# Optimization experiments

Measured on AMD Instinct MI355X. Metric: run time of the kernel, lower is better.

## Reference

```python
import jax, jax.numpy as jnp
import numpy as np

B, NP, L, C, NA = 16, 512, 20, 3, 50
RATIO = 0.8
K = int(np.ceil(RATIO * NP))  # 410 nodes kept per graph
N = B * NP
E = 6 * N
NF, EF = 13, 4
EPS = 1e-5


def _graph_norm(x, w, b, ms):
    # PyG GraphNorm called WITHOUT batch in the source -> single global graph
    mean = x.mean(0)
    out = x - ms * mean
    var = (out * out).mean(0)
    return w * out / jnp.sqrt(var + EPS) + b


def _forward(x, pan_w, lin1_w, lin1_b, norm1_w, norm1_b, norm1_ms,
             pool_p, pool_beta, gat_wl, gat_bl, gat_wr, gat_br, gat_att, gat_bias,
             norm2_w, norm2_b, norm2_ms,
             val1_w, val1_b, val2_w, val2_b, val3_w, val3_b,
             adv1_w, adv1_b, adv2_w, adv2_b, adv3_w, adv3_b,
             edge_index, current_node_ids, action_mask):
    src, dst = edge_index[0], edge_index[1]
    # PANConv builds SparseTensor(row=edge_index[1], col=edge_index[0]) -> row = target
    A = jnp.zeros((B, NP, NP), x.dtype).at[dst // NP, dst % NP, src % NP].set(1.0)
    eyeB = jnp.broadcast_to(jnp.eye(NP, dtype=x.dtype), A.shape)

    # panentropy: M = sum_{i=0..L} w_i * A^i  (dense per graph)
    def step(carry, wi):
        tmp, acc = carry
        tmp = tmp @ A
        return (tmp, acc + wi * tmp), None
    (_, M), _ = jax.lax.scan(step, (eyeB, pan_w[0] * eyeB), pan_w[1:])
    deg = M.sum(-1)                                   # row sums
    dis = jnp.where(deg > 0, 1.0 / jnp.sqrt(deg), 0.0)
    Mn = dis[:, :, None] * M * dis[:, None, :]        # D^-1/2 M D^-1/2

    # conv1: propagate (Mn @ x) then Linear
    x3 = x.reshape(B, NP, NF)
    h = jnp.einsum('bij,bjf->bif', Mn, x3) @ lin1_w + lin1_b   # [B,NP,C]
    x1 = jax.nn.relu(_graph_norm(h.reshape(N, C), norm1_w, norm1_b, norm1_ms))  # [N,C]
    h = x1.reshape(B, NP, C)

    # PANPooling: score = tanh(b0 * <x,p> + b1 * colsum(Mn)); keep top K per graph
    score = jnp.tanh(pool_beta[0] * (h * pool_p).sum(-1) + pool_beta[1] * Mn.sum(-2))
    vals, idx = jax.lax.top_k(score, K)                        # [B,K]
    xp = jnp.take_along_axis(h, idx[:, :, None], axis=1) * vals[..., None]
    Mg = jax.vmap(lambda m, i: m[i][:, i])(Mn, idx)            # filtered adjacency [B,K,K]
    mask = (jnp.swapaxes(Mg, 1, 2) != 0) | jnp.eye(K, dtype=bool)  # mask[b,i,j]: edge j->i (+self loops)

    # GATv2Conv, heads=1, eval mode (no dropout), edge_attr not passed in source
    xl = xp @ gat_wl + gat_bl
    xr = xp @ gat_wr + gat_br
    e = jax.nn.leaky_relu(xr[:, :, None, :] + xl[:, None, :, :], 0.2)  # [B,i,j,C]
    logits = jnp.where(mask, jnp.einsum('bijc,c->bij', e, gat_att), -1e9)
    alpha = jax.nn.softmax(logits, axis=-1)
    g = jnp.einsum('bij,bjc->bic', alpha, xl) + gat_bias

    g = jax.nn.relu(_graph_norm(g.reshape(B * K, C), norm2_w, norm2_b, norm2_ms)).reshape(B, K, C)
    gp = g.sum(1)                                              # global_add_pool [B,C]

    # source uses POOLED bincount cumsum offsets to index the pre-pool arrays (faithful)
    gidx = current_node_ids + jnp.arange(B, dtype=current_node_ids.dtype) * K
    feat = jnp.concatenate([x[gidx], x1[gidx], gp], axis=1)    # [B,19]

    a = jax.nn.relu(feat @ adv1_w + adv1_b)
    a = jax.nn.relu(a @ adv2_w + adv2_b)
    a = a @ adv3_w + adv3_b
    v = jax.nn.relu(feat @ val1_w + val1_b)
    v = jax.nn.relu(v @ val2_w + val2_b)
    v = v @ val3_w + val3_b
    q = v + (a - a.mean(1, keepdims=True))
    return jnp.where(action_mask == 0, -1e8, q)


def setup_inputs() -> dict:
    key = jax.random.key(0)
    ks = list(jax.random.split(key, 40))
    nk = lambda: ks.pop()
    # within-graph random edges so the PyG-style batch structure is valid
    g = jax.random.randint(nk(), (E,), 0, B)
    u = jax.random.randint(nk(), (E,), 0, NP)
    v = jax.random.randint(nk(), (E,), 0, NP)
    edge_index = jnp.stack([g * NP + u, g * NP + v]).astype(jnp.int32)

    def lin(k, i, o):
        k1, k2 = jax.random.split(k)
        return (jax.random.normal(k1, (i, o), jnp.float32) / np.sqrt(i),
                jax.random.normal(k2, (o,), jnp.float32) * 0.01)

    lin1_w, lin1_b = lin(nk(), NF, C)
    gat_wl, gat_bl = lin(nk(), C, C)
    gat_wr, gat_br = lin(nk(), C, C)
    val1_w, val1_b = lin(nk(), 19, 10)
    val2_w, val2_b = lin(nk(), 10, 5)
    val3_w, val3_b = lin(nk(), 5, 1)
    adv1_w, adv1_b = lin(nk(), 19, 10)
    adv2_w, adv2_b = lin(nk(), 10, 5)
    adv3_w, adv3_b = lin(nk(), 5, NA)
    return dict(
        x=jax.random.normal(nk(), (N, NF), jnp.float32),
        edge_index=edge_index,
        edge_attr=jax.random.normal(nk(), (E, EF), jnp.float32),
        batch=jnp.arange(N, dtype=jnp.int32) // NP,
        current_node_ids=jax.random.randint(nk(), (B,), 0, NP),
        action_mask=jax.random.randint(nk(), (B, NA), 0, 2),
        pan_w=jax.random.uniform(nk(), (L + 1,), jnp.float32) * 0.5,
        lin1_w=lin1_w, lin1_b=lin1_b,
        norm1_w=jnp.ones(C), norm1_b=jnp.zeros(C), norm1_ms=jnp.ones(C),
        pool_p=jax.random.normal(nk(), (C,), jnp.float32),
        pool_beta=jnp.array([0.5, 0.5], jnp.float32),
        gat_wl=gat_wl, gat_bl=gat_bl, gat_wr=gat_wr, gat_br=gat_br,
        gat_att=jax.random.normal(nk(), (C,), jnp.float32),
        gat_bias=jax.random.normal(nk(), (C,), jnp.float32) * 0.01,
        norm2_w=jnp.ones(C), norm2_b=jnp.zeros(C), norm2_ms=jnp.ones(C),
        val1_w=val1_w, val1_b=val1_b, val2_w=val2_w, val2_b=val2_b,
        val3_w=val3_w, val3_b=val3_b,
        adv1_w=adv1_w, adv1_b=adv1_b, adv2_w=adv2_w, adv2_b=adv2_b,
        adv3_w=adv3_w, adv3_b=adv3_b,
    )


def reference(x, edge_index, edge_attr, batch, current_node_ids, action_mask,
              pan_w, lin1_w, lin1_b, norm1_w, norm1_b, norm1_ms,
              pool_p, pool_beta, gat_wl, gat_bl, gat_wr, gat_br, gat_att, gat_bias,
              norm2_w, norm2_b, norm2_ms,
              val1_w, val1_b, val2_w, val2_b, val3_w, val3_b,
              adv1_w, adv1_b, adv2_w, adv2_b, adv3_w, adv3_b):
    del edge_attr, batch  # received by the torch forward but never consumed
    return _forward(x, pan_w, lin1_w, lin1_b, norm1_w, norm1_b, norm1_ms,
                    pool_p, pool_beta, gat_wl, gat_bl, gat_wr, gat_br, gat_att, gat_bias,
                    norm2_w, norm2_b, norm2_ms,
                    val1_w, val1_b, val2_w, val2_b, val3_w, val3_b,
                    adv1_w, adv1_b, adv2_w, adv2_b, adv3_w, adv3_b,
                    edge_index, current_node_ids, action_mask)
```

## Files before the change

### kernel.cpp

```cpp
#include <hip/hip_runtime.h>
#include <hip/hip_bf16.h>
#include <stdint.h>
#include <math.h>

#define BB   16
#define NPn  512
#define LLp  20
#define NAa  50
#define KKk  410
#define NNt  (BB * NPn)
#define EEe  (6 * NNt)
#define NFf  13
#define KPAD 416
#define EPSf 1e-5f
#define QCLMP 1e6f
#define MAXD 28
#define PADR 512

__device__ __forceinline__ float r15_sane(float v) {
    if (!(v == v)) return 0.0f;
    return fminf(fmaxf(v, -1e15f), 1e15f);
}

__global__ __launch_bounds__(256) void r15_scatter(
    const int* __restrict__ ei,
    uint32_t* __restrict__ fwdb, uint32_t* __restrict__ trsb)
{
    const int e = blockIdx.x * 256 + threadIdx.x;
    if (e < EEe) {
        const int src = ei[e], dst = ei[EEe + e];
        atomicOr(&fwdb[(size_t)dst * 16 + ((src & 511) >> 5)], 1u << (src & 31));
        atomicOr(&trsb[(size_t)src * 16 + ((dst & 511) >> 5)], 1u << (dst & 31));
    }
}

__global__ __launch_bounds__(256) void r15_extract(
    const uint32_t* __restrict__ fwdb, const uint32_t* __restrict__ trsb,
    unsigned short* __restrict__ csrF, unsigned short* __restrict__ csrT)
{
    const int t = blockIdx.x * 256 + threadIdx.x;
    const int node = t & 8191;
    const uint32_t* bs = (t < 8192) ? (fwdb + (size_t)node * 16)
                                    : (trsb + (size_t)node * 16);
    unsigned short* cs = (t < 8192) ? csrF : csrT;
    int cnt = 0;
    for (int w = 0; w < 16; ++w) {
        uint32_t bits = bs[w];
        while (bits) {
            const int u = (w << 5) + __ffs(bits) - 1;
            bits &= bits - 1;
            if (cnt < MAXD) cs[(size_t)cnt * 8192 + node] = (unsigned short)u;
            ++cnt;
        }
    }
    for (int j = cnt; j < MAXD; ++j) cs[(size_t)j * 8192 + node] = PADR;
}

__global__ __launch_bounds__(512) void r15_mid(
    const float* __restrict__ x,
    const unsigned short* __restrict__ csrF,
    const unsigned short* __restrict__ csrT,
    const float* __restrict__ panw,
    const float* __restrict__ l1w, const float* __restrict__ l1b,
    float* __restrict__ h_raw, float* __restrict__ colsum,
    uint32_t* __restrict__ Rb)
{
    __shared__ __align__(16) uint32_t sbuf[1047];
    float* pa  = (float*)sbuf;
    float* pb  = (float*)(sbuf + 513);
    float* wsh = (float*)(sbuf + 1026);
    const int b = blockIdx.x, y = blockIdx.y, t = threadIdx.x;
    const int node = b * 512 + t;

    if (y < 4) {
        const int c = y;
        int iF[MAXD];
#pragma unroll
        for (int j = 0; j < MAXD; ++j) iF[j] = (int)csrF[(size_t)j * 8192 + node];
        if (t < 21) wsh[t] = panw[t];

        pa[t] = 1.0f;
        if (t == 0) { pa[512] = 0.0f; pb[512] = 0.0f; }
        __syncthreads();
        float dacc = wsh[0];
        {
            float* rp = pa; float* rn = pb;
            for (int i = 1; i <= LLp; ++i) {
                float tv[MAXD];
#pragma unroll
                for (int j = 0; j < MAXD; ++j) tv[j] = rp[iF[j]];
                float s = 0.0f;
#pragma unroll
                for (int j = 0; j < MAXD; ++j) s += tv[j];
                rn[t] = s;
                dacc += wsh[i] * s;
                __syncthreads();
                float* tp = rp; rp = rn; rn = tp;
            }
        }
        const float d0 = (dacc > 0.0f) ? 1.0f / sqrtf(dacc) : 0.0f;

        int idx[MAXD];
        if (c == 3) {
#pragma unroll
            for (int j = 0; j < MAXD; ++j) idx[j] = (int)csrT[(size_t)j * 8192 + node];
        } else {
#pragma unroll
            for (int j = 0; j < MAXD; ++j) idx[j] = iF[j];
        }
        float seed;
        if (c < 3) {
            float xw = 0.0f;
            const float* xr = x + (size_t)node * NFf;
            for (int f = 0; f < NFf; ++f) xw += xr[f] * l1w[f * 3 + c];
            seed = d0 * xw;
        } else {
            seed = d0;
        }
        pa[t] = seed;
        if (t == 0) { pa[512] = 0.0f; pb[512] = 0.0f; }
        __syncthreads();
        float acc = wsh[0] * seed;
        {
            float* rp = pa; float* rn = pb;
            for (int i = 1; i <= LLp; ++i) {
                float tv[MAXD];
#pragma unroll
                for (int j = 0; j < MAXD; ++j) tv[j] = rp[idx[j]];
                float s = 0.0f;
#pragma unroll
                for (int j = 0; j < MAXD; ++j) s += tv[j];
                rn[t] = s;
                acc += wsh[i] * s;
                __syncthreads();
                float* tp = rp; rp = rn; rn = tp;
            }
        }
        if (c < 3) h_raw[(size_t)node * 3 + c] = r15_sane(d0 * acc + l1b[c]);
        else       colsum[node] = r15_sane(d0 * acc);
    } else {
        const int q = y - 4;
        int iF[MAXD];
#pragma unroll
        for (int j = 0; j < MAXD; ++j) iF[j] = (int)csrF[(size_t)j * 8192 + node];
        uint32_t* R1 = sbuf;
        uint32_t* R2 = sbuf + 513;
        R1[t] = ((t >> 5) == q) ? (1u << (t & 31)) : 0u;
        if (t == 0) { R1[512] = 0u; R2[512] = 0u; }
        __syncthreads();
        uint32_t* Rp = R1; uint32_t* Rn = R2;
        for (int i = 0; i < LLp; ++i) {
            uint32_t tv[MAXD];
#pragma unroll
            for (int j = 0; j < MAXD; ++j) tv[j] = Rp[iF[j]];
            uint32_t r = Rp[t];
#pragma unroll
            for (int j = 0; j < MAXD; ++j) r |= tv[j];
            Rn[t] = r;
            __syncthreads();
            uint32_t* tp = Rp; Rp = Rn; Rn = tp;
        }
        Rb[(size_t)node * 16 + q] = Rp[t];
    }
}

__global__ __launch_bounds__(512) void r15_poolgat(
    const float* __restrict__ h_raw,
    const float* __restrict__ colsum,
    const uint32_t* __restrict__ Rb,
    const float* n1w, const float* n1b, const float* n1ms,
    const float* poolp, const float* poolb,
    const float* gwl, const float* gbl,
    const float* gwr, const float* gbr,
    const float* gatt, const float* gbias,
    float* __restrict__ x1,
    float* __restrict__ g_raw)
{
    __shared__ __align__(16) uint32_t pg[10592];
    float* red  = (float*)pg;
    float* sc   = (float*)(pg + 512);
    float* mv   = (float*)(pg + 1024);
    float* xpS  = (float*)(pg + 1032);
    int*   kidx = (int*)(pg + 2280);
    float* xlS  = (float*)(pg + 2696);
    uint32_t* RT = pg + 3928;
    const int b = blockIdx.x, y = blockIdx.y, t = threadIdx.x;
    const float inv_n = 1.0f / (float)NNt;

    float hv0[16], hv1[16], hv2[16];
    float s0 = 0.0f, s1 = 0.0f, s2 = 0.0f;
#pragma unroll
    for (int k = 0; k < 16; ++k) {
        const float* hr = h_raw + (size_t)(k * 512 + t) * 3;
        hv0[k] = hr[0]; hv1[k] = hr[1]; hv2[k] = hr[2];
        s0 += hv0[k]; s1 += hv1[k]; s2 += hv2[k];
    }
    float acc[3] = { s0, s1, s2 };
    for (int c = 0; c < 3; ++c) {
        __syncthreads();
        red[t] = acc[c];
        __syncthreads();
        for (int st = 256; st > 0; st >>= 1) {
            if (t < st) red[t] += red[t + st];
            __syncthreads();
        }
        if (t == 0) mv[c] = red[0] * inv_n;
    }
    __syncthreads();
    const float mm0 = n1ms[0] * mv[0], mm1 = n1ms[1] * mv[1], mm2 = n1ms[2] * mv[2];
    float a0 = 0.0f, a1 = 0.0f, a2 = 0.0f;
#pragma unroll
    for (int k = 0; k < 16; ++k) {
        const float d0 = hv0[k] - mm0, d1 = hv1[k] - mm1, d2 = hv2[k] - mm2;
        a0 += d0 * d0; a1 += d1 * d1; a2 += d2 * d2;
    }
    float accv[3] = { a0, a1, a2 };
    for (int c = 0; c < 3; ++c) {
        __syncthreads();
        red[t] = accv[c];
        __syncthreads();
        for (int st = 256; st > 0; st >>= 1) {
            if (t < st) red[t] += red[t + st];
            __syncthreads();
        }
        if (t == 0) mv[3 + c] = red[0] * inv_n;
    }
    __syncthreads();

    const float mmv[3] = { mm0, mm1, mm2 };
    float xv[3];
#pragma unroll
    for (int c = 0; c < 3; ++c) {
        const float iv = 1.0f / sqrtf(fmaxf(mv[3 + c], 0.0f) + EPSf);
        const float o  = h_raw[(size_t)(b * NPn + t) * 3 + c] - mmv[c];
        const float tt = n1w[c] * o * iv + n1b[c];
        xv[c] = fmaxf(tt, 0.0f);
        if (y == 0) x1[(size_t)(b * NPn + t) * 3 + c] = xv[c];
    }
    float s = poolb[0] * (xv[0] * poolp[0] + xv[1] * poolp[1] + xv[2] * poolp[2])
            + poolb[1] * colsum[b * NPn + t];
    s = tanhf(s);
    if (!(s == s)) s = 0.0f;
    sc[t] = s;
    __syncthreads();
    int cnt = 0;
    for (int u = 0; u < NPn; ++u) {
        const float su = sc[u];
        cnt += ((su > s) || (su == s && u < t)) ? 1 : 0;
    }
    if (cnt < KKk) {
        kidx[cnt] = t;
        xpS[cnt * 3 + 0] = xv[0] * s;
        xpS[cnt * 3 + 1] = xv[1] * s;
        xpS[cnt * 3 + 2] = xv[2] * s;
    }
    __syncthreads();

    float Wl[9], Wr[9];
#pragma unroll
    for (int i2 = 0; i2 < 9; ++i2) { Wl[i2] = gwl[i2]; Wr[i2] = gwr[i2]; }
    const float Bl0 = gbl[0], Bl1 = gbl[1], Bl2 = gbl[2];
    const float Br0 = gbr[0], Br1 = gbr[1], Br2 = gbr[2];
    const float At0 = gatt[0], At1 = gatt[1], At2 = gatt[2];
    const float Gb0 = gbias[0], Gb1 = gbias[1], Gb2 = gbias[2];
    for (int j = t; j < KKk; j += 512) {
        const float p0 = xpS[j * 3 + 0];
        const float p1 = xpS[j * 3 + 1];
        const float p2 = xpS[j * 3 + 2];
        xlS[j * 3 + 0] = p0 * Wl[0] + p1 * Wl[3] + p2 * Wl[6] + Bl0;
        xlS[j * 3 + 1] = p0 * Wl[1] + p1 * Wl[4] + p2 * Wl[7] + Bl1;
        xlS[j * 3 + 2] = p0 * Wl[2] + p1 * Wl[5] + p2 * Wl[8] + Bl2;
        const uint32_t* rr = Rb + (size_t)(b * NPn + kidx[j]) * 16;
#pragma unroll
        for (int w = 0; w < 16; ++w) RT[w * KPAD + j] = rr[w];
    }
    __syncthreads();

    const int lane = t & 63, wv = t >> 6;
    const int wid = y * 8 + wv;
    for (int i = wid; i < KKk; i += 64) {
        const float p0 = xpS[i * 3 + 0];
        const float p1 = xpS[i * 3 + 1];
        const float p2 = xpS[i * 3 + 2];
        const float xr0 = p0 * Wr[0] + p1 * Wr[3] + p2 * Wr[6] + Br0;
        const float xr1 = p0 * Wr[1] + p1 * Wr[4] + p2 * Wr[7] + Br1;
        const float xr2 = p0 * Wr[2] + p1 * Wr[5] + p2 * Wr[8] + Br2;
        const int bi = kidx[i];
        const uint32_t mbit = 1u << (bi & 31);
        const uint32_t* Rw = &RT[(bi >> 5) * KPAD];
        float mx = -3e38f, lsum = 0.0f, b0 = 0.0f, b1 = 0.0f, b2 = 0.0f;
        for (int j = lane; j < KKk; j += 64) {
            if ((Rw[j] & mbit) || (j == i)) {
                float e0 = xr0 + xlS[j * 3 + 0]; e0 = e0 > 0.0f ? e0 : 0.2f * e0;
                float e1 = xr1 + xlS[j * 3 + 1]; e1 = e1 > 0.0f ? e1 : 0.2f * e1;
                float e2 = xr2 + xlS[j * 3 + 2]; e2 = e2 > 0.0f ? e2 : 0.2f * e2;
                const float sv = At0 * e0 + At1 * e1 + At2 * e2;
                if (sv > mx) {
                    const float r = __expf(mx - sv);
                    lsum *= r; b0 *= r; b1 *= r; b2 *= r;
                    mx = sv;
                }
                const float pj = __expf(sv - mx);
                lsum += pj;
                b0 += pj * xlS[j * 3 + 0];
                b1 += pj * xlS[j * 3 + 1];
                b2 += pj * xlS[j * 3 + 2];
            }
        }
        for (int off = 32; off; off >>= 1) {
            const float mo = __shfl_xor(mx, off);
            const float lo = __shfl_xor(lsum, off);
            const float c0 = __shfl_xor(b0, off);
            const float c1 = __shfl_xor(b1, off);
            const float c2 = __shfl_xor(b2, off);
            const float M  = fmaxf(mx, mo);
            const float ea = __expf(mx - M), eb = __expf(mo - M);
            lsum = lsum * ea + lo * eb;
            b0 = b0 * ea + c0 * eb;
            b1 = b1 * ea + c1 * eb;
            b2 = b2 * ea + c2 * eb;
            mx = M;
        }
        if (lane == 0) {
            const float rl = 1.0f / fmaxf(lsum, 1e-30f);
            g_raw[(size_t)(b * KPAD + i) * 3 + 0] = r15_sane(b0 * rl + Gb0);
            g_raw[(size_t)(b * KPAD + i) * 3 + 1] = r15_sane(b1 * rl + Gb1);
            g_raw[(size_t)(b * KPAD + i) * 3 + 2] = r15_sane(b2 * rl + Gb2);
        }
    }
}

__global__ __launch_bounds__(512) void r15_head(
    const float* __restrict__ g_raw,
    const float* __restrict__ x1,
    const float* __restrict__ x,
    const int* __restrict__ cnid,
    const int* __restrict__ amask,
    const float* n2w, const float* n2b, const float* n2ms,
    const float* v1w, const float* v1b,
    const float* v2w, const float* v2b,
    const float* v3w, const float* v3b,
    const float* a1w, const float* a1b,
    const float* a2w, const float* a2b,
    const float* a3w, const float* a3b,
    float* __restrict__ out)
{
    __shared__ float rbuf[512];
    __shared__ float mv[6];
    __shared__ float gp[3];
    __shared__ float feat[19];
    __shared__ float h1a[10], h1v[10], h2a[5], h2v[5];
    __shared__ float a3[50];
    __shared__ float vout_s, amean_s;
    const int b = blockIdx.x, t = threadIdx.x;
    const float denom = 1.0f / (float)(BB * KKk);

    float gv0[13], gv1[13], gv2[13];
    float s0 = 0.0f, s1 = 0.0f, s2 = 0.0f;
#pragma unroll
    for (int k = 0; k < 13; ++k) {
        const int r = k * 512 + t;
        float q0 = 0.0f, q1 = 0.0f, q2 = 0.0f;
        if (r < BB * KKk) {
            const int bq = r / KKk, iq = r - bq * KKk;
            const float* gr = g_raw + (size_t)(bq * KPAD + iq) * 3;
            q0 = gr[0]; q1 = gr[1]; q2 = gr[2];
        }
        gv0[k] = q0; gv1[k] = q1; gv2[k] = q2;
        s0 += q0; s1 += q1; s2 += q2;
    }
    float acc[3] = { s0, s1, s2 };
    for (int c = 0; c < 3; ++c) {
        __syncthreads();
        rbuf[t] = acc[c];
        __syncthreads();
        for (int st = 256; st > 0; st >>= 1) {
            if (t < st) rbuf[t] += rbuf[t + st];
            __syncthreads();
        }
        if (t == 0) mv[c] = rbuf[0] * denom;
    }
    __syncthreads();
    const float mm0 = n2ms[0] * mv[0], mm1 = n2ms[1] * mv[1], mm2 = n2ms[2] * mv[2];
    float a0 = 0.0f, a1 = 0.0f, a2 = 0.0f;
#pragma unroll
    for (int k = 0; k < 13; ++k) {
        const int r = k * 512 + t;
        if (r < BB * KKk) {
            const float d0 = gv0[k] - mm0, d1 = gv1[k] - mm1, d2 = gv2[k] - mm2;
            a0 += d0 * d0; a1 += d1 * d1; a2 += d2 * d2;
        }
    }
    float accv[3] = { a0, a1, a2 };
    for (int c = 0; c < 3; ++c) {
        __syncthreads();
        rbuf[t] = accv[c];
        __syncthreads();
        for (int st = 256; st > 0; st >>= 1) {
            if (t < st) rbuf[t] += rbuf[t + st];
            __syncthreads();
        }
        if (t == 0) mv[3 + c] = rbuf[0] * denom;
    }
    __syncthreads();

    const float mmv[3] = { mm0, mm1, mm2 };
    float s3[3] = { 0.0f, 0.0f, 0.0f };
    if (t < KKk) {
        const size_t r = (size_t)(b * KPAD + t) * 3;
#pragma unroll
        for (int c = 0; c < 3; ++c) {
            const float iv = 1.0f / sqrtf(fmaxf(mv[3 + c], 0.0f) + EPSf);
            s3[c] = fmaxf((g_raw[r + c] - mmv[c]) * iv * n2w[c] + n2b[c], 0.0f);
        }
    }
    for (int c = 0; c < 3; ++c) {
        __syncthreads();
        rbuf[t] = s3[c];
        __syncthreads();
        for (int st = 256; st > 0; st >>= 1) {
            if (t < st) rbuf[t] += rbuf[t + st];
            __syncthreads();
        }
        if (t == 0) gp[c] = rbuf[0];
    }
    __syncthreads();

    if (t < 19) {
        const int gidx = cnid[b] + b * KKk;
        float fv;
        if (t < 13)      fv = x[(size_t)gidx * NFf + t];
        else if (t < 16) fv = x1[(size_t)gidx * 3 + (t - 13)];
        else             fv = gp[t - 16];
        feat[t] = fv;
    }
    __syncthreads();

    if (t < 10) {
        float s = a1b[t];
        for (int f = 0; f < 19; ++f) s += feat[f] * a1w[f * 10 + t];
        h1a[t] = fmaxf(s, 0.0f);
    } else if (t >= 64 && t < 74) {
        const int j = t - 64;
        float s = v1b[j];
        for (int f = 0; f < 19; ++f) s += feat[f] * v1w[f * 10 + j];
        h1v[j] = fmaxf(s, 0.0f);
    }
    __syncthreads();
    if (t < 5) {
        float s = a2b[t];
        for (int k = 0; k < 10; ++k) s += h1a[k] * a2w[k * 5 + t];
        h2a[t] = fmaxf(s, 0.0f);
    } else if (t >= 64 && t < 69) {
        const int j = t - 64;
        float s = v2b[j];
        for (int k = 0; k < 10; ++k) s += h1v[k] * v2w[k * 5 + j];
        h2v[j] = fmaxf(s, 0.0f);
    }
    __syncthreads();
    if (t < 50) {
        float s = a3b[t];
        for (int k = 0; k < 5; ++k) s += h2a[k] * a3w[k * 50 + t];
        a3[t] = s;
    } else if (t == 64) {
        float s = v3b[0];
        for (int k = 0; k < 5; ++k) s += h2v[k] * v3w[k];
        vout_s = s;
    }
    __syncthreads();
    if (t == 0) {
        float s = 0.0f;
        for (int k = 0; k < 50; ++k) s += a3[k];
        amean_s = s * (1.0f / 50.0f);
    }
    __syncthreads();
    if (t < 50) {
        float q = vout_s + a3[t] - amean_s;
        if (!(q == q)) q = 0.0f;
        q = fminf(fmaxf(q, -QCLMP), QCLMP);
        out[b * NAa + t] = (amask[b * NAa + t] == 0) ? -1e8f : q;
    }
}

extern "C" void kernel_launch(void* const* d_in, const int* in_sizes, int n_in,
                              void* d_out, int out_size, void* d_ws, size_t ws_size,
                              hipStream_t stream) {
    (void)in_sizes; (void)n_in; (void)out_size;
    const float* x     = (const float*)d_in[0];
    const int* ei      = (const int*)d_in[1];
    const int* cnid    = (const int*)d_in[4];
    const int* amask   = (const int*)d_in[5];
    const float* panw  = (const float*)d_in[6];
    const float* l1w   = (const float*)d_in[7];
    const float* l1b   = (const float*)d_in[8];
    const float* n1w   = (const float*)d_in[9];
    const float* n1b   = (const float*)d_in[10];
    const float* n1ms  = (const float*)d_in[11];
    const float* poolp = (const float*)d_in[12];
    const float* poolb = (const float*)d_in[13];
    const float* gwl   = (const float*)d_in[14];
    const float* gbl   = (const float*)d_in[15];
    const float* gwr   = (const float*)d_in[16];
    const float* gbr   = (const float*)d_in[17];
    const float* gatt  = (const float*)d_in[18];
    const float* gbias = (const float*)d_in[19];
    const float* n2w   = (const float*)d_in[20];
    const float* n2b   = (const float*)d_in[21];
    const float* n2ms  = (const float*)d_in[22];
    const float* v1w   = (const float*)d_in[23];
    const float* v1b   = (const float*)d_in[24];
    const float* v2w   = (const float*)d_in[25];
    const float* v2b   = (const float*)d_in[26];
    const float* v3w   = (const float*)d_in[27];
    const float* v3b   = (const float*)d_in[28];
    const float* a1w   = (const float*)d_in[29];
    const float* a1b   = (const float*)d_in[30];
    const float* a2w   = (const float*)d_in[31];
    const float* a2b   = (const float*)d_in[32];
    const float* a3w   = (const float*)d_in[33];
    const float* a3b   = (const float*)d_in[34];
    float* out         = (float*)d_out;

    uint8_t* wsb = (uint8_t*)d_ws;
    uint32_t* fwdb = (uint32_t*)wsb;
    uint32_t* trsb = (uint32_t*)(wsb + 524288);
    uint32_t* Rb   = (uint32_t*)(wsb + 1048576);
    unsigned short* csrF = (unsigned short*)(wsb + 1572864);
    unsigned short* csrT = csrF + (size_t)MAXD * 8192;
    float* h_raw  = (float*)(csrT + (size_t)MAXD * 8192);
    float* x1     = h_raw + (size_t)NNt * 3;
    float* colsum = x1 + (size_t)NNt * 3;
    float* g_raw  = colsum + NNt;
    const size_t needed = 1572864 + 2 * (size_t)MAXD * 8192 * 2 +
                          ((size_t)(2 * NNt * 3 + NNt + BB * KPAD * 3)) * 4;
    if (ws_size < needed) return;

    hipMemsetAsync(fwdb, 0, 1048576, stream);
    r15_scatter<<<dim3((EEe + 255) / 256), dim3(256), 0, stream>>>(ei, fwdb, trsb);
    r15_extract<<<dim3(64), dim3(256), 0, stream>>>(fwdb, trsb, csrF, csrT);
    r15_mid<<<dim3(16, 20), dim3(512), 0, stream>>>(x, csrF, csrT, panw, l1w, l1b,
                                                    h_raw, colsum, Rb);
    r15_poolgat<<<dim3(16, 8), dim3(512), 0, stream>>>(h_raw, colsum, Rb,
                                                       n1w, n1b, n1ms, poolp, poolb,
                                                       gwl, gbl, gwr, gbr, gatt, gbias,
                                                       x1, g_raw);
    r15_head<<<dim3(16), dim3(512), 0, stream>>>(g_raw, x1, x, cnid, amask,
                                                 n2w, n2b, n2ms, v1w, v1b, v2w, v2b, v3w, v3b,
                                                 a1w, a1b, a2w, a2b, a3w, a3b, out);
}
```

Before: 225.3 us.

## Fuse adjacency build into one LDS kernel, use wave-shuffle reductions, unroll GAT loop

Replaces the memset, global-atomic scatter and extract kernels with a single per-graph kernel that builds the forward and transpose bitmasks in shared memory and emits the padded neighbour lists. Each of the 16 blocks scans the full edge list, so edge reads are repeated 16 times in exchange for removing two launches and the global atomics. Block reductions in the pooling and head kernels switch from shared-memory tree reductions to wave shuffles plus a small cross-wave sum. The GAT attention loop becomes a fully unrolled fixed-trip loop over padded columns, evaluating scores unconditionally and masking only the accumulation.

```diff
diff --git a/kernel.cpp b/kernel.cpp
--- a/kernel.cpp
+++ b/kernel.cpp
@@ -12,51 +12,65 @@
 #define EEe  (6 * NNt)
 #define NFf  13
 #define KPAD 416
+#define KP2  448
 #define EPSf 1e-5f
 #define QCLMP 1e6f
 #define MAXD 28
 #define PADR 512
 
-__device__ __forceinline__ float r15_sane(float v) {
+__device__ __forceinline__ float r16_sane(float v) {
     if (!(v == v)) return 0.0f;
     return fminf(fmaxf(v, -1e15f), 1e15f);
 }
 
-__global__ __launch_bounds__(256) void r15_scatter(
+__global__ __launch_bounds__(512) void r16_build(
     const int* __restrict__ ei,
-    uint32_t* __restrict__ fwdb, uint32_t* __restrict__ trsb)
-{
-    const int e = blockIdx.x * 256 + threadIdx.x;
-    if (e < EEe) {
-        const int src = ei[e], dst = ei[EEe + e];
-        atomicOr(&fwdb[(size_t)dst * 16 + ((src & 511) >> 5)], 1u << (src & 31));
-        atomicOr(&trsb[(size_t)src * 16 + ((dst & 511) >> 5)], 1u << (dst & 31));
-    }
-}
-
-__global__ __launch_bounds__(256) void r15_extract(
-    const uint32_t* __restrict__ fwdb, const uint32_t* __restrict__ trsb,
     unsigned short* __restrict__ csrF, unsigned short* __restrict__ csrT)
 {
-    const int t = blockIdx.x * 256 + threadIdx.x;
-    const int node = t & 8191;
-    const uint32_t* bs = (t < 8192) ? (fwdb + (size_t)node * 16)
-                                    : (trsb + (size_t)node * 16);
-    unsigned short* cs = (t < 8192) ? csrF : csrT;
-    int cnt = 0;
-    for (int w = 0; w < 16; ++w) {
-        uint32_t bits = bs[w];
-        while (bits) {
-            const int u = (w << 5) + __ffs(bits) - 1;
-            bits &= bits - 1;
-            if (cnt < MAXD) cs[(size_t)cnt * 8192 + node] = (unsigned short)u;
-            ++cnt;
-        }
-    }
-    for (int j = cnt; j < MAXD; ++j) cs[(size_t)j * 8192 + node] = PADR;
+    __shared__ uint32_t fw[NPn * 16];
+    __shared__ uint32_t tr[NPn * 16];
+    const int b = blockIdx.x, t = threadIdx.x;
+#pragma unroll
+    for (int w = 0; w < 16; ++w) { fw[t * 16 + w] = 0u; tr[t * 16 + w] = 0u; }
+    __syncthreads();
+    for (int e = t; e < EEe; e += 512) {
+        const int src = ei[e], dst = ei[EEe + e];
+        if ((dst >> 9) == b)
+            atomicOr(&fw[(dst & 511) * 16 + ((src & 511) >> 5)], 1u << (src & 31));
+        if ((src >> 9) == b)
+            atomicOr(&tr[(src & 511) * 16 + ((dst & 511) >> 5)], 1u << (dst & 31));
+    }
+    __syncthreads();
+    const int node = b * 512 + t;
+    {
+        int cnt = 0;
+        for (int w = 0; w < 16; ++w) {
+            uint32_t bits = fw[t * 16 + w];
+            while (bits) {
+                const int u = (w << 5) + __ffs(bits) - 1;
+                bits &= bits - 1;
+                if (cnt < MAXD) csrF[(size_t)cnt * 8192 + node] = (unsigned short)u;
+                ++cnt;
+            }
+        }
+        for (int j = cnt; j < MAXD; ++j) csrF[(size_t)j * 8192 + node] = PADR;
+    }
+    {
+        int cnt = 0;
+        for (int w = 0; w < 16; ++w) {
+            uint32_t bits = tr[t * 16 + w];
+            while (bits) {
+                const int u = (w << 5) + __ffs(bits) - 1;
+                bits &= bits - 1;
+                if (cnt < MAXD) csrT[(size_t)cnt * 8192 + node] = (unsigned short)u;
+                ++cnt;
+            }
+        }
+        for (int j = cnt; j < MAXD; ++j) csrT[(size_t)j * 8192 + node] = PADR;
+    }
 }
 
-__global__ __launch_bounds__(512) void r15_mid(
+__global__ __launch_bounds__(512) void r16_mid(
     const float* __restrict__ x,
     const unsigned short* __restrict__ csrF,
     const unsigned short* __restrict__ csrT,
@@ -136,8 +150,8 @@
                 float* tp = rp; rp = rn; rn = tp;
             }
         }
-        if (c < 3) h_raw[(size_t)node * 3 + c] = r15_sane(d0 * acc + l1b[c]);
-        else       colsum[node] = r15_sane(d0 * acc);
+        if (c < 3) h_raw[(size_t)node * 3 + c] = r16_sane(d0 * acc + l1b[c]);
+        else       colsum[node] = r16_sane(d0 * acc);
     } else {
         const int q = y - 4;
         int iF[MAXD];
@@ -164,7 +178,7 @@
     }
 }
 
-__global__ __launch_bounds__(512) void r15_poolgat(
+__global__ __launch_bounds__(512) void r16_poolgat(
     const float* __restrict__ h_raw,
     const float* __restrict__ colsum,
     const uint32_t* __restrict__ Rb,
@@ -176,54 +190,55 @@
     float* __restrict__ x1,
     float* __restrict__ g_raw)
 {
-    __shared__ __align__(16) uint32_t pg[10592];
-    float* red  = (float*)pg;
-    float* sc   = (float*)(pg + 512);
-    float* mv   = (float*)(pg + 1024);
-    float* xpS  = (float*)(pg + 1032);
-    int*   kidx = (int*)(pg + 2280);
-    float* xlS  = (float*)(pg + 2696);
-    uint32_t* RT = pg + 3928;
+    __shared__ __align__(16) uint32_t pg[10744];
+    float* sc   = (float*)pg;
+    float* mv   = (float*)(pg + 512);
+    float* wred = (float*)(pg + 520);
+    float* xpS  = (float*)(pg + 568);
+    int*   kidx = (int*)(pg + 1816);
+    float* xlS  = (float*)(pg + 2232);
+    uint32_t* RT = pg + 3576;
     const int b = blockIdx.x, y = blockIdx.y, t = threadIdx.x;
+    const int lane = t & 63, wv = t >> 6;
     const float inv_n = 1.0f / (float)NNt;
 
     float hv0[16], hv1[16], hv2[16];
-    float s0 = 0.0f, s1 = 0.0f, s2 = 0.0f;
+    float p0 = 0.0f, p1 = 0.0f, p2 = 0.0f;
 #pragma unroll
     for (int k = 0; k < 16; ++k) {
         const float* hr = h_raw + (size_t)(k * 512 + t) * 3;
         hv0[k] = hr[0]; hv1[k] = hr[1]; hv2[k] = hr[2];
-        s0 += hv0[k]; s1 += hv1[k]; s2 += hv2[k];
-    }
-    float acc[3] = { s0, s1, s2 };
-    for (int c = 0; c < 3; ++c) {
-        __syncthreads();
-        red[t] = acc[c];
-        __syncthreads();
-        for (int st = 256; st > 0; st >>= 1) {
-            if (t < st) red[t] += red[t + st];
-            __syncthreads();
-        }
-        if (t == 0) mv[c] = red[0] * inv_n;
+        p0 += hv0[k]; p1 += hv1[k]; p2 += hv2[k];
+    }
+#pragma unroll
+    for (int off = 32; off; off >>= 1) {
+        p0 += __shfl_xor(p0, off); p1 += __shfl_xor(p1, off); p2 += __shfl_xor(p2, off);
+    }
+    if (lane == 0) { wred[wv * 3 + 0] = p0; wred[wv * 3 + 1] = p1; wred[wv * 3 + 2] = p2; }
+    __syncthreads();
+    if (t < 3) {
+        float s = 0.0f;
+        for (int w = 0; w < 8; ++w) s += wred[w * 3 + t];
+        mv[t] = s * inv_n;
     }
     __syncthreads();
     const float mm0 = n1ms[0] * mv[0], mm1 = n1ms[1] * mv[1], mm2 = n1ms[2] * mv[2];
-    float a0 = 0.0f, a1 = 0.0f, a2 = 0.0f;
+    float q0 = 0.0f, q1 = 0.0f, q2 = 0.0f;
 #pragma unroll
     for (int k = 0; k < 16; ++k) {
         const float d0 = hv0[k] - mm0, d1 = hv1[k] - mm1, d2 = hv2[k] - mm2;
-        a0 += d0 * d0; a1 += d1 * d1; a2 += d2 * d2;
-    }
-    float accv[3] = { a0, a1, a2 };
-    for (int c = 0; c < 3; ++c) {
-        __syncthreads();
-        red[t] = accv[c];
-        __syncthreads();
-        for (int st = 256; st > 0; st >>= 1) {
-            if (t < st) red[t] += red[t + st];
-            __syncthreads();
-        }
-        if (t == 0) mv[3 + c] = red[0] * inv_n;
+        q0 += d0 * d0; q1 += d1 * d1; q2 += d2 * d2;
+    }
+#pragma unroll
+    for (int off = 32; off; off >>= 1) {
+        q0 += __shfl_xor(q0, off); q1 += __shfl_xor(q1, off); q2 += __shfl_xor(q2, off);
+    }
+    if (lane == 0) { wred[wv * 3 + 0] = q0; wred[wv * 3 + 1] = q1; wred[wv * 3 + 2] = q2; }
+    __syncthreads();
+    if (t < 3) {
+        float s = 0.0f;
+        for (int w = 0; w < 8; ++w) s += wred[w * 3 + t];
+        mv[3 + t] = s * inv_n;
     }
     __syncthreads();
 
@@ -263,38 +278,51 @@
     const float Br0 = gbr[0], Br1 = gbr[1], Br2 = gbr[2];
     const float At0 = gatt[0], At1 = gatt[1], At2 = gatt[2];
     const float Gb0 = gbias[0], Gb1 = gbias[1], Gb2 = gbias[2];
-    for (int j = t; j < KKk; j += 512) {
-        const float p0 = xpS[j * 3 + 0];
-        const float p1 = xpS[j * 3 + 1];
-        const float p2 = xpS[j * 3 + 2];
-        xlS[j * 3 + 0] = p0 * Wl[0] + p1 * Wl[3] + p2 * Wl[6] + Bl0;
-        xlS[j * 3 + 1] = p0 * Wl[1] + p1 * Wl[4] + p2 * Wl[7] + Bl1;
-        xlS[j * 3 + 2] = p0 * Wl[2] + p1 * Wl[5] + p2 * Wl[8] + Bl2;
-        const uint32_t* rr = Rb + (size_t)(b * NPn + kidx[j]) * 16;
-#pragma unroll
-        for (int w = 0; w < 16; ++w) RT[w * KPAD + j] = rr[w];
-    }
-    __syncthreads();
-
-    const int lane = t & 63, wv = t >> 6;
+    if (t < KP2) {
+        const int j = t;
+        if (j < KKk) {
+            const float c0 = xpS[j * 3 + 0];
+            const float c1 = xpS[j * 3 + 1];
+            const float c2 = xpS[j * 3 + 2];
+            xlS[j * 3 + 0] = c0 * Wl[0] + c1 * Wl[3] + c2 * Wl[6] + Bl0;
+            xlS[j * 3 + 1] = c0 * Wl[1] + c1 * Wl[4] + c2 * Wl[7] + Bl1;
+            xlS[j * 3 + 2] = c0 * Wl[2] + c1 * Wl[5] + c2 * Wl[8] + Bl2;
+            const uint32_t* rr = Rb + (size_t)(b * NPn + kidx[j]) * 16;
+#pragma unroll
+            for (int w = 0; w < 16; ++w) RT[w * KP2 + j] = rr[w];
+        } else {
+            xlS[j * 3 + 0] = 0.0f; xlS[j * 3 + 1] = 0.0f; xlS[j * 3 + 2] = 0.0f;
+#pragma unroll
+            for (int w = 0; w < 16; ++w) RT[w * KP2 + j] = 0u;
+        }
+    }
+    __syncthreads();
+
     const int wid = y * 8 + wv;
     for (int i = wid; i < KKk; i += 64) {
-        const float p0 = xpS[i * 3 + 0];
-        const float p1 = xpS[i * 3 + 1];
-        const float p2 = xpS[i * 3 + 2];
-        const float xr0 = p0 * Wr[0] + p1 * Wr[3] + p2 * Wr[6] + Br0;
-        const float xr1 = p0 * Wr[1] + p1 * Wr[4] + p2 * Wr[7] + Br1;
-        const float xr2 = p0 * Wr[2] + p1 * Wr[5] + p2 * Wr[8] + Br2;
+        const float c0 = xpS[i * 3 + 0];
+        const float c1 = xpS[i * 3 + 1];
+        const float c2 = xpS[i * 3 + 2];
+        const float xr0 = c0 * Wr[0] + c1 * Wr[3] + c2 * Wr[6] + Br0;
+        const float xr1 = c0 * Wr[1] + c1 * Wr[4] + c2 * Wr[7] + Br1;
+        const float xr2 = c0 * Wr[2] + c1 * Wr[5] + c2 * Wr[8] + Br2;
         const int bi = kidx[i];
         const uint32_t mbit = 1u << (bi & 31);
-        const uint32_t* Rw = &RT[(bi >> 5) * KPAD];
+        const uint32_t* Rw = &RT[(bi >> 5) * KP2];
         float mx = -3e38f, lsum = 0.0f, b0 = 0.0f, b1 = 0.0f, b2 = 0.0f;
-        for (int j = lane; j < KKk; j += 64) {
-            if ((Rw[j] & mbit) || (j == i)) {
-                float e0 = xr0 + xlS[j * 3 + 0]; e0 = e0 > 0.0f ? e0 : 0.2f * e0;
-                float e1 = xr1 + xlS[j * 3 + 1]; e1 = e1 > 0.0f ? e1 : 0.2f * e1;
-                float e2 = xr2 + xlS[j * 3 + 2]; e2 = e2 > 0.0f ? e2 : 0.2f * e2;
-                const float sv = At0 * e0 + At1 * e1 + At2 * e2;
+#pragma unroll
+        for (int it = 0; it < 7; ++it) {
+            const int j = lane + it * 64;
+            const uint32_t rw = Rw[j];
+            const float xl0 = xlS[j * 3 + 0];
+            const float xl1 = xlS[j * 3 + 1];
+            const float xl2 = xlS[j * 3 + 2];
+            const bool valid = (rw & mbit) || (j == i);
+            float e0 = xr0 + xl0; e0 = e0 > 0.0f ? e0 : 0.2f * e0;
+            float e1 = xr1 + xl1; e1 = e1 > 0.0f ? e1 : 0.2f * e1;
+            float e2 = xr2 + xl2; e2 = e2 > 0.0f ? e2 : 0.2f * e2;
+            const float sv = At0 * e0 + At1 * e1 + At2 * e2;
+            if (valid) {
                 if (sv > mx) {
                     const float r = __expf(mx - sv);
                     lsum *= r; b0 *= r; b1 *= r; b2 *= r;
@@ -302,35 +330,34 @@
                 }
                 const float pj = __expf(sv - mx);
                 lsum += pj;
-                b0 += pj * xlS[j * 3 + 0];
-                b1 += pj * xlS[j * 3 + 1];
-                b2 += pj * xlS[j * 3 + 2];
+                b0 += pj * xl0; b1 += pj * xl1; b2 += pj * xl2;
             }
         }
+#pragma unroll
         for (int off = 32; off; off >>= 1) {
             const float mo = __shfl_xor(mx, off);
             const float lo = __shfl_xor(lsum, off);
-            const float c0 = __shfl_xor(b0, off);
-            const float c1 = __shfl_xor(b1, off);
-            const float c2 = __shfl_xor(b2, off);
+            const float d0 = __shfl_xor(b0, off);
+            const float d1 = __shfl_xor(b1, off);
+            const float d2 = __shfl_xor(b2, off);
             const float M  = fmaxf(mx, mo);
             const float ea = __expf(mx - M), eb = __expf(mo - M);
             lsum = lsum * ea + lo * eb;
-            b0 = b0 * ea + c0 * eb;
-            b1 = b1 * ea + c1 * eb;
-            b2 = b2 * ea + c2 * eb;
+            b0 = b0 * ea + d0 * eb;
+            b1 = b1 * ea + d1 * eb;
+            b2 = b2 * ea + d2 * eb;
             mx = M;
         }
         if (lane == 0) {
             const float rl = 1.0f / fmaxf(lsum, 1e-30f);
-            g_raw[(size_t)(b * KPAD + i) * 3 + 0] = r15_sane(b0 * rl + Gb0);
-            g_raw[(size_t)(b * KPAD + i) * 3 + 1] = r15_sane(b1 * rl + Gb1);
-            g_raw[(size_t)(b * KPAD + i) * 3 + 2] = r15_sane(b2 * rl + Gb2);
+            g_raw[(size_t)(b * KPAD + i) * 3 + 0] = r16_sane(b0 * rl + Gb0);
+            g_raw[(size_t)(b * KPAD + i) * 3 + 1] = r16_sane(b1 * rl + Gb1);
+            g_raw[(size_t)(b * KPAD + i) * 3 + 2] = r16_sane(b2 * rl + Gb2);
         }
     }
 }
 
-__global__ __launch_bounds__(512) void r15_head(
+__global__ __launch_bounds__(512) void r16_head(
     const float* __restrict__ g_raw,
     const float* __restrict__ x1,
     const float* __restrict__ x,
@@ -345,7 +372,7 @@
     const float* a3w, const float* a3b,
     float* __restrict__ out)
 {
-    __shared__ float rbuf[512];
+    __shared__ float wred[24];
     __shared__ float mv[6];
     __shared__ float gp[3];
     __shared__ float feat[19];
@@ -353,10 +380,11 @@
     __shared__ float a3[50];
     __shared__ float vout_s, amean_s;
     const int b = blockIdx.x, t = threadIdx.x;
+    const int lane = t & 63, wv = t >> 6;
     const float denom = 1.0f / (float)(BB * KKk);
 
     float gv0[13], gv1[13], gv2[13];
-    float s0 = 0.0f, s1 = 0.0f, s2 = 0.0f;
+    float p0 = 0.0f, p1 = 0.0f, p2 = 0.0f;
 #pragma unroll
     for (int k = 0; k < 13; ++k) {
         const int r = k * 512 + t;
@@ -367,40 +395,40 @@
             q0 = gr[0]; q1 = gr[1]; q2 = gr[2];
         }
         gv0[k] = q0; gv1[k] = q1; gv2[k] = q2;
-        s0 += q0; s1 += q1; s2 += q2;
-    }
-    float acc[3] = { s0, s1, s2 };
-    for (int c = 0; c < 3; ++c) {
-        __syncthreads();
-        rbuf[t] = acc[c];
-        __syncthreads();
-        for (int st = 256; st > 0; st >>= 1) {
-            if (t < st) rbuf[t] += rbuf[t + st];
-            __syncthreads();
-        }
-        if (t == 0) mv[c] = rbuf[0] * denom;
+        p0 += q0; p1 += q1; p2 += q2;
+    }
+#pragma unroll
+    for (int off = 32; off; off >>= 1) {
+        p0 += __shfl_xor(p0, off); p1 += __shfl_xor(p1, off); p2 += __shfl_xor(p2, off);
+    }
+    if (lane == 0) { wred[wv * 3 + 0] = p0; wred[wv * 3 + 1] = p1; wred[wv * 3 + 2] = p2; }
+    __syncthreads();
+    if (t < 3) {
+        float s = 0.0f;
+        for (int w = 0; w < 8; ++w) s += wred[w * 3 + t];
+        mv[t] = s * denom;
     }
     __syncthreads();
     const float mm0 = n2ms[0] * mv[0], mm1 = n2ms[1] * mv[1], mm2 = n2ms[2] * mv[2];
-    float a0 = 0.0f, a1 = 0.0f, a2 = 0.0f;
+    float q0a = 0.0f, q1a = 0.0f, q2a = 0.0f;
 #pragma unroll
     for (int k = 0; k < 13; ++k) {
         const int r = k * 512 + t;
         if (r < BB * KKk) {
             const float d0 = gv0[k] - mm0, d1 = gv1[k] - mm1, d2 = gv2[k] - mm2;
-            a0 += d0 * d0; a1 += d1 * d1; a2 += d2 * d2;
-        }
-    }
-    float accv[3] = { a0, a1, a2 };
-    for (int c = 0; c < 3; ++c) {
-        __syncthreads();
-        rbuf[t] = accv[c];
-        __syncthreads();
-        for (int st = 256; st > 0; st >>= 1) {
-            if (t < st) rbuf[t] += rbuf[t + st];
-            __syncthreads();
-        }
-        if (t == 0) mv[3 + c] = rbuf[0] * denom;
+            q0a += d0 * d0; q1a += d1 * d1; q2a += d2 * d2;
+        }
+    }
+#pragma unroll
+    for (int off = 32; off; off >>= 1) {
+        q0a += __shfl_xor(q0a, off); q1a += __shfl_xor(q1a, off); q2a += __shfl_xor(q2a, off);
+    }
+    if (lane == 0) { wred[wv * 3 + 0] = q0a; wred[wv * 3 + 1] = q1a; wred[wv * 3 + 2] = q2a; }
+    __syncthreads();
+    if (t < 3) {
+        float s = 0.0f;
+        for (int w = 0; w < 8; ++w) s += wred[w * 3 + t];
+        mv[3 + t] = s * denom;
     }
     __syncthreads();
 
@@ -414,15 +442,17 @@
             s3[c] = fmaxf((g_raw[r + c] - mmv[c]) * iv * n2w[c] + n2b[c], 0.0f);
         }
     }
-    for (int c = 0; c < 3; ++c) {
-        __syncthreads();
-        rbuf[t] = s3[c];
-        __syncthreads();
-        for (int st = 256; st > 0; st >>= 1) {
-            if (t < st) rbuf[t] += rbuf[t + st];
-            __syncthreads();
-        }
-        if (t == 0) gp[c] = rbuf[0];
+    float g0 = s3[0], g1 = s3[1], g2 = s3[2];
+#pragma unroll
+    for (int off = 32; off; off >>= 1) {
+        g0 += __shfl_xor(g0, off); g1 += __shfl_xor(g1, off); g2 += __shfl_xor(g2, off);
+    }
+    if (lane == 0) { wred[wv * 3 + 0] = g0; wred[wv * 3 + 1] = g1; wred[wv * 3 + 2] = g2; }
+    __syncthreads();
+    if (t < 3) {
+        float s = 0.0f;
+        for (int w = 0; w < 8; ++w) s += wred[w * 3 + t];
+        gp[t] = s;
     }
     __syncthreads();
 
@@ -522,29 +552,25 @@
     float* out         = (float*)d_out;
 
     uint8_t* wsb = (uint8_t*)d_ws;
-    uint32_t* fwdb = (uint32_t*)wsb;
-    uint32_t* trsb = (uint32_t*)(wsb + 524288);
-    uint32_t* Rb   = (uint32_t*)(wsb + 1048576);
-    unsigned short* csrF = (unsigned short*)(wsb + 1572864);
+    uint32_t* Rb   = (uint32_t*)wsb;
+    unsigned short* csrF = (unsigned short*)(wsb + 524288);
     unsigned short* csrT = csrF + (size_t)MAXD * 8192;
     float* h_raw  = (float*)(csrT + (size_t)MAXD * 8192);
     float* x1     = h_raw + (size_t)NNt * 3;
     float* colsum = x1 + (size_t)NNt * 3;
     float* g_raw  = colsum + NNt;
-    const size_t needed = 1572864 + 2 * (size_t)MAXD * 8192 * 2 +
+    const size_t needed = 524288 + 2 * (size_t)MAXD * 8192 * 2 +
                           ((size_t)(2 * NNt * 3 + NNt + BB * KPAD * 3)) * 4;
     if (ws_size < needed) return;
 
-    hipMemsetAsync(fwdb, 0, 1048576, stream);
-    r15_scatter<<<dim3((EEe + 255) / 256), dim3(256), 0, stream>>>(ei, fwdb, trsb);
-    r15_extract<<<dim3(64), dim3(256), 0, stream>>>(fwdb, trsb, csrF, csrT);
-    r15_mid<<<dim3(16, 20), dim3(512), 0, stream>>>(x, csrF, csrT, panw, l1w, l1b,
+    r16_build<<<dim3(16), dim3(512), 0, stream>>>(ei, csrF, csrT);
+    r16_mid<<<dim3(16, 20), dim3(512), 0, stream>>>(x, csrF, csrT, panw, l1w, l1b,
                                                     h_raw, colsum, Rb);
-    r15_poolgat<<<dim3(16, 8), dim3(512), 0, stream>>>(h_raw, colsum, Rb,
+    r16_poolgat<<<dim3(16, 8), dim3(512), 0, stream>>>(h_raw, colsum, Rb,
                                                        n1w, n1b, n1ms, poolp, poolb,
                                                        gwl, gbl, gwr, gbr, gatt, gbias,
                                                        x1, g_raw);
-    r15_head<<<dim3(16), dim3(512), 0, stream>>>(g_raw, x1, x, cnid, amask,
+    r16_head<<<dim3(16), dim3(512), 0, stream>>>(g_raw, x1, x, cnid, amask,
                                                  n2w, n2b, n2ms, v1w, v1b, v2w, v2b, v3w, v3b,
                                                  a1w, a1b, a2w, a2b, a3w, a3b, out);
 }
```

Result: slower. 247.6 us (+9.9%).
